# Optimization experiments

Measured on AMD Instinct MI355X. Metric: run time of the kernel, lower is better.

Reference implementation:

```python
import jax, jax.numpy as jnp
import numpy as np
import math

N_EMBD = 64
HEAD_SIZE = 64
B, T = 16, 2048


def setup_inputs() -> dict:
    key = jax.random.key(0)
    k1, k2, k3, k4 = jax.random.split(key, 4)
    inputs = jax.random.normal(k1, (B, T, N_EMBD), dtype=jnp.float32)
    # Causal mask: True where attention is NOT allowed (upper triangle),
    # matching masked_fill_(mask, -1e9) with mask = ~tril.
    mask = jnp.triu(jnp.ones((T, T), dtype=bool), k=1)
    # nn.Linear(n_embd, head_size, bias=False) weights, stored as
    # (n_embd, head_size) so projection is inputs @ W (== x @ W_torch.T).
    scale = 1.0 / math.sqrt(N_EMBD)
    Wq = jax.random.uniform(k2, (N_EMBD, HEAD_SIZE), jnp.float32, -scale, scale)
    Wk = jax.random.uniform(k3, (N_EMBD, HEAD_SIZE), jnp.float32, -scale, scale)
    Wv = jax.random.uniform(k4, (N_EMBD, HEAD_SIZE), jnp.float32, -scale, scale)
    return {"inputs": inputs, "mask": mask, "Wq": Wq, "Wk": Wk, "Wv": Wv}


def reference(inputs, mask, Wq, Wk, Wv):
    # inputs: (B, T, n_embd); mask: (T, T) bool broadcast over batch
    q = inputs @ Wq  # (B, T, H)
    k = inputs @ Wk  # (B, T, H)
    v = inputs @ Wv  # (B, T, H)
    inv_sqrt_h = 1.0 / math.sqrt(HEAD_SIZE)
    scores = jnp.einsum('bth,bsh->bts', q, k) * inv_sqrt_h  # (B, T, T)
    scores = jnp.where(mask, jnp.float32(-1e9), scores)
    attention = jax.nn.softmax(scores, axis=-1)
    out = jnp.einsum('bts,bsh->bth', attention, v)  # (B, T, H)
    return out
```

## Files before the change

### kernel.cpp

```cpp
#include <hip/hip_runtime.h>
#include <stdint.h>


typedef __bf16 bf16x8 __attribute__((ext_vector_type(8)));
typedef __bf16 bf16x4 __attribute__((ext_vector_type(4)));
typedef float f32x4 __attribute__((ext_vector_type(4)));

#define QSCALE 0.18033688011112042f

#if __has_builtin(__builtin_amdgcn_exp2f)
#define EXP2(x) __builtin_amdgcn_exp2f(x)
#else
#define EXP2(x) exp2f(x)
#endif

__device__ __forceinline__ unsigned short f2bf(float f) {
  union { float f; unsigned u; } x; x.f = f;
  unsigned r = x.u + 0x7fffu + ((x.u >> 16) & 1u);
  return (unsigned short)(r >> 16);
}

__device__ __forceinline__ int swz(int row, int bytecol) {
  return row * 128 + (bytecol ^ ((row & 7) << 4));
}
__device__ __forceinline__ bf16x8 frag(const unsigned short* base, int row, int kf, int lane) {
  int off = swz(row, kf * 64 + ((lane >> 4) << 4));
  return *(const bf16x8*)((const char*)base + off);
}

__global__ __launch_bounds__(256, 2) void proj_kernel(
    const float* __restrict__ X, const float* __restrict__ Wq,
    const float* __restrict__ Wk, const float* __restrict__ Wv,
    unsigned short* __restrict__ Qg, unsigned short* __restrict__ Kg,
    unsigned short* __restrict__ Vtg) {
  __shared__ __align__(16) unsigned short Xs[128 * 64];
  __shared__ __align__(16) unsigned short Ws[3 * 64 * 64];
  const int tid = threadIdx.x, lane = tid & 63, w = tid >> 6;
  const long grow0 = (long)blockIdx.x * 128;

  for (int c = tid; c < 1024; c += 256) {
    int r = c >> 3, cc = c & 7;
    const float* src = X + (grow0 + r) * 64 + cc * 8;
    float4 f0 = *(const float4*)src;
    float4 f1 = *(const float4*)(src + 4);
    uint4 d;
    d.x = f2bf(f0.x) | ((unsigned)f2bf(f0.y) << 16);
    d.y = f2bf(f0.z) | ((unsigned)f2bf(f0.w) << 16);
    d.z = f2bf(f1.x) | ((unsigned)f2bf(f1.y) << 16);
    d.w = f2bf(f1.z) | ((unsigned)f2bf(f1.w) << 16);
    *(uint4*)((char*)Xs + swz(r, cc * 16)) = d;
  }
  for (int c = tid; c < 3 * 4096; c += 256) {
    const int mat = c >> 12;
    const int rr = c & 4095;
    const int e = rr >> 6, hh = rr & 63;
    const float* wsrc = (mat == 0) ? Wq : (mat == 1) ? Wk : Wv;
    *(unsigned short*)((char*)(Ws + mat * 4096) + swz(hh, e * 2)) = f2bf(wsrc[e * 64 + hh]);
  }
  __syncthreads();

  const f32x4 zero = {0.f, 0.f, 0.f, 0.f};
  const int mrowb = w * 32;

  bf16x8 xf[2][2];
#pragma unroll
  for (int s = 0; s < 2; ++s)
#pragma unroll
    for (int kf = 0; kf < 2; ++kf)
      xf[s][kf] = frag(Xs, mrowb + s * 16 + (lane & 15), kf, lane);

#pragma unroll
  for (int mat = 0; mat < 2; ++mat) {
    unsigned short* dst = mat ? Kg : Qg;
    const unsigned short* wbase = Ws + mat * 4096;
#pragma unroll
    for (int s = 0; s < 2; ++s) {
#pragma unroll
      for (int nt = 0; nt < 4; ++nt) {
        bf16x8 b0 = frag(wbase, nt * 16 + (lane & 15), 0, lane);
        bf16x8 b1 = frag(wbase, nt * 16 + (lane & 15), 1, lane);
        f32x4 acc = __builtin_amdgcn_mfma_f32_16x16x32_bf16(xf[s][0], b0, zero, 0, 0, 0);
        acc = __builtin_amdgcn_mfma_f32_16x16x32_bf16(xf[s][1], b1, acc, 0, 0, 0);
        long row0 = grow0 + mrowb + s * 16 + ((lane >> 4) << 2);
        int col = nt * 16 + (lane & 15);
#pragma unroll
        for (int i = 0; i < 4; ++i) {
          float v = acc[i];
          if (mat == 0) v *= QSCALE;
          dst[(row0 + i) * 64 + col] = f2bf(v);
        }
      }
    }
  }

  const unsigned short* wv = Ws + 2 * 4096;
  const int b = (int)(grow0 >> 11);
  const int tin0 = (int)(grow0 & 2047);
#pragma unroll
  for (int mt = 0; mt < 4; ++mt) {
    bf16x8 a0 = frag(wv, mt * 16 + (lane & 15), 0, lane);
    bf16x8 a1 = frag(wv, mt * 16 + (lane & 15), 1, lane);
#pragma unroll
    for (int s = 0; s < 2; ++s) {
      f32x4 acc = __builtin_amdgcn_mfma_f32_16x16x32_bf16(a0, xf[s][0], zero, 0, 0, 0);
      acc = __builtin_amdgcn_mfma_f32_16x16x32_bf16(a1, xf[s][1], acc, 0, 0, 0);
      int t = tin0 + mrowb + s * 16 + (lane & 15);
      int h0 = mt * 16 + ((lane >> 4) << 2);
#pragma unroll
      for (int i = 0; i < 4; ++i)
        Vtg[((long)(b * 64 + h0 + i)) * 2048 + t] = f2bf(acc[i]);
    }
  }
}

__global__ __launch_bounds__(256, 4) void attn3_kernel(
    const unsigned short* __restrict__ Qg, const unsigned short* __restrict__ Kg,
    const unsigned short* __restrict__ Vtg, float* __restrict__ Og) {
  __shared__ __align__(16) unsigned char smem[32768];

  const int bid = blockIdx.x;
  const int slot = bid >> 3;
  const int b = ((bid & 7) << 1) + (slot & 1);
  const int j = slot >> 1;
  const int qt = (j & 1) ? (j >> 1) : 63 - (j >> 1);
  const int q0 = qt * 32;

  const int tid = threadIdx.x;
  const int lane = tid & 63, w = tid >> 6;
  const int g = lane >> 4, ln = lane & 15;
  const int h = w & 1, qs = w >> 1;

  const int ns = (q0 + 95) >> 6;

  const unsigned short* qrow = Qg + ((long)b * 2048 + q0 + qs * 16 + ln) * 64;
  const bf16x8 qb0 = *(const bf16x8*)(qrow + g * 8);
  const bf16x8 qb1 = *(const bf16x8*)(qrow + 32 + g * 8);

  const unsigned short* kbase = Kg + (long)b * 2048 * 64;
  const unsigned short* vbase = Vtg + (long)b * 64 * 2048;

  const int sr = tid >> 2;
  const int sc = tid & 3;

  const f32x4 zero = {0.f, 0.f, 0.f, 0.f};
  f32x4 oacc[4];
#pragma unroll
  for (int nt = 0; nt < 4; ++nt) oacc[nt] = zero;
  float den = 0.f;

  {
    const unsigned short* kg = kbase + (long)sr * 64 + sc * 16;
    uint4 k0 = *(const uint4*)kg;
    uint4 k1 = *(const uint4*)(kg + 8);
    const unsigned short* vg = vbase + (long)sr * 2048 + sc * 16;
    uint4 v0 = *(const uint4*)vg;
    uint4 v1 = *(const uint4*)(vg + 8);
    unsigned short* Kb = (unsigned short*)smem;
    unsigned short* Vb = (unsigned short*)(smem + 8192);
    *(uint4*)((char*)Kb + swz(sr, sc * 32)) = k0;
    *(uint4*)((char*)Kb + swz(sr, sc * 32 + 16)) = k1;
    *(uint4*)((char*)Vb + swz(sr, sc * 32)) = v0;
    *(uint4*)((char*)Vb + swz(sr, sc * 32 + 16)) = v1;
  }
  __syncthreads();

  int cur = 0;
  for (int t = 0; t < ns; ++t) {
    const bool pre = (t + 1 < ns);
    uint4 k0, k1, v0, v1;
    if (pre) {
      const int kv0n = (t + 1) * 64;
      const unsigned short* kg = kbase + (long)(kv0n + sr) * 64 + sc * 16;
      k0 = *(const uint4*)kg;
      k1 = *(const uint4*)(kg + 8);
      const unsigned short* vg = vbase + (long)sr * 2048 + kv0n + sc * 16;
      v0 = *(const uint4*)vg;
      v1 = *(const uint4*)(vg + 8);
    }

    const unsigned short* Kb = (const unsigned short*)(smem + cur * 16384);
    const unsigned short* Vb = (const unsigned short*)(smem + cur * 16384 + 8192);

    bf16x8 ka00 = frag(Kb, h * 32 + ln,      0, lane);
    bf16x8 ka01 = frag(Kb, h * 32 + ln,      1, lane);
    bf16x8 ka10 = frag(Kb, h * 32 + 16 + ln, 0, lane);
    bf16x8 ka11 = frag(Kb, h * 32 + 16 + ln, 1, lane);

    bf16x8 vb[4];
#pragma unroll
    for (int nt = 0; nt < 4; ++nt) {
      int row = nt * 16 + ln;
      bf16x4 lo = *(const bf16x4*)((const char*)Vb + swz(row, h * 64 + g * 8));
      bf16x4 hi = *(const bf16x4*)((const char*)Vb + swz(row, h * 64 + 32 + g * 8));
      vb[nt] = __builtin_shufflevector(lo, hi, 0, 1, 2, 3, 4, 5, 6, 7);
    }

    __builtin_amdgcn_s_setprio(1);
    f32x4 st0 = __builtin_amdgcn_mfma_f32_16x16x32_bf16(ka00, qb0, zero, 0, 0, 0);
    st0 = __builtin_amdgcn_mfma_f32_16x16x32_bf16(ka01, qb1, st0, 0, 0, 0);
    f32x4 st1 = __builtin_amdgcn_mfma_f32_16x16x32_bf16(ka10, qb0, zero, 0, 0, 0);
    st1 = __builtin_amdgcn_mfma_f32_16x16x32_bf16(ka11, qb1, st1, 0, 0, 0);
    __builtin_amdgcn_s_setprio(0);

    if (t == ns - 1) {
      const int qglob = q0 + qs * 16 + ln;
      const int kvb = t * 64 + h * 32 + g * 4;
#pragma unroll
      for (int i = 0; i < 4; ++i) {
        if (kvb + i > qglob) st0[i] = -1e30f;
        if (kvb + 16 + i > qglob) st1[i] = -1e30f;
      }
    }

    bf16x8 pa;
#pragma unroll
    for (int i = 0; i < 4; ++i) {
      float p0 = EXP2(st0[i]);
      float p1 = EXP2(st1[i]);
      den += p0 + p1;
      pa[i] = (__bf16)p0;
      pa[4 + i] = (__bf16)p1;
    }

    __builtin_amdgcn_s_setprio(1);
#pragma unroll
    for (int nt = 0; nt < 4; ++nt)
      oacc[nt] = __builtin_amdgcn_mfma_f32_16x16x32_bf16(pa, vb[nt], oacc[nt], 0, 0, 0);
    __builtin_amdgcn_s_setprio(0);

    if (pre) {
      unsigned short* Kn = (unsigned short*)(smem + (cur ^ 1) * 16384);
      unsigned short* Vn = (unsigned short*)(smem + (cur ^ 1) * 16384 + 8192);
      *(uint4*)((char*)Kn + swz(sr, sc * 32)) = k0;
      *(uint4*)((char*)Kn + swz(sr, sc * 32 + 16)) = k1;
      *(uint4*)((char*)Vn + swz(sr, sc * 32)) = v0;
      *(uint4*)((char*)Vn + swz(sr, sc * 32 + 16)) = v1;
    }
    __syncthreads();
    cur ^= 1;
  }

  den += __shfl_xor(den, 16);
  den += __shfl_xor(den, 32);

  float* Olds = (float*)smem;
  float* Dlds = (float*)(smem + 4 * 16 * 68 * 4);
#pragma unroll
  for (int nt = 0; nt < 4; ++nt)
#pragma unroll
    for (int i = 0; i < 4; ++i)
      Olds[(w * 16 + g * 4 + i) * 68 + nt * 16 + ln] = oacc[nt][i];
  if (lane < 16) Dlds[w * 16 + ln] = den;
  __syncthreads();

  const int q32 = tid >> 3;
  const int r = q32 & 15, qsx = q32 >> 4;
  const int d0 = (tid & 7) * 8;
  float dd = Dlds[(qsx * 2) * 16 + r] + Dlds[(qsx * 2 + 1) * 16 + r];
  float inv = 1.0f / dd;
  float acc[8];
#pragma unroll
  for (int e = 0; e < 8; ++e)
    acc[e] = (Olds[((qsx * 2) * 16 + r) * 68 + d0 + e] +
              Olds[((qsx * 2 + 1) * 16 + r) * 68 + d0 + e]) * inv;
  float* outp = Og + ((long)b * 2048 + q0 + q32) * 64 + d0;
  *(float4*)outp = make_float4(acc[0], acc[1], acc[2], acc[3]);
  *(float4*)(outp + 4) = make_float4(acc[4], acc[5], acc[6], acc[7]);
}

extern "C" void kernel_launch(void* const* d_in, const int* in_sizes, int n_in,
                              void* d_out, int out_size, void* d_ws, size_t ws_size,
                              hipStream_t stream) {
  const float* X  = (const float*)d_in[0];
  const float* Wq = (const float*)d_in[2];
  const float* Wk = (const float*)d_in[3];
  const float* Wv = (const float*)d_in[4];

  unsigned short* Qg  = (unsigned short*)d_ws;
  unsigned short* Kg  = Qg + 2097152;
  unsigned short* Vtg = Kg + 2097152;

  proj_kernel<<<256, 256, 0, stream>>>(X, Wq, Wk, Wv, Qg, Kg, Vtg);
  attn3_kernel<<<1024, 256, 0, stream>>>(Qg, Kg, Vtg, (float*)d_out);
}
```

Before: 46.67 us.

## Split KV range across waves with per-wave async K loads and split projection grid

The attention kernel now gives each wave its own strided subset of 32-key tiles, covering all 32 queries, instead of splitting by query half and key half. K tiles are staged with per-wave global_load_lds double buffering and V is read straight from global memory into registers, which drops the block-wide __syncthreads in the loop. Partial outputs and denominators from the four waves are merged through LDS at the end. The projection kernel runs one block per weight matrix (grid y=3) for more parallelism, at the cost of converting X three times. The exp2 builtin is also replaced by exp2f. Risks include uncoalesced V loads and hand-set vmcnt waits.

```diff
diff --git a/kernel.cpp b/kernel.cpp
--- a/kernel.cpp
+++ b/kernel.cpp
@@ -7,12 +7,6 @@
 typedef float f32x4 __attribute__((ext_vector_type(4)));
 
 #define QSCALE 0.18033688011112042f
-
-#if __has_builtin(__builtin_amdgcn_exp2f)
-#define EXP2(x) __builtin_amdgcn_exp2f(x)
-#else
-#define EXP2(x) exp2f(x)
-#endif
 
 __device__ __forceinline__ unsigned short f2bf(float f) {
   union { float f; unsigned u; } x; x.f = f;
@@ -28,14 +22,21 @@
   return *(const bf16x8*)((const char*)base + off);
 }
 
-__global__ __launch_bounds__(256, 2) void proj_kernel(
+__device__ __forceinline__ void gload_lds16(const unsigned short* g, unsigned short* l) {
+  __builtin_amdgcn_global_load_lds(
+      (const __attribute__((address_space(1))) unsigned int*)g,
+      (__attribute__((address_space(3))) unsigned int*)l, 16, 0, 0);
+}
+
+__global__ __launch_bounds__(256, 3) void proj_kernel(
     const float* __restrict__ X, const float* __restrict__ Wq,
     const float* __restrict__ Wk, const float* __restrict__ Wv,
     unsigned short* __restrict__ Qg, unsigned short* __restrict__ Kg,
     unsigned short* __restrict__ Vtg) {
   __shared__ __align__(16) unsigned short Xs[128 * 64];
-  __shared__ __align__(16) unsigned short Ws[3 * 64 * 64];
+  __shared__ __align__(16) unsigned short Ws[64 * 64];
   const int tid = threadIdx.x, lane = tid & 63, w = tid >> 6;
+  const int mat = blockIdx.y;
   const long grow0 = (long)blockIdx.x * 128;
 
   for (int c = tid; c < 1024; c += 256) {
@@ -50,12 +51,10 @@
     d.w = f2bf(f1.z) | ((unsigned)f2bf(f1.w) << 16);
     *(uint4*)((char*)Xs + swz(r, cc * 16)) = d;
   }
-  for (int c = tid; c < 3 * 4096; c += 256) {
-    const int mat = c >> 12;
-    const int rr = c & 4095;
-    const int e = rr >> 6, hh = rr & 63;
-    const float* wsrc = (mat == 0) ? Wq : (mat == 1) ? Wk : Wv;
-    *(unsigned short*)((char*)(Ws + mat * 4096) + swz(hh, e * 2)) = f2bf(wsrc[e * 64 + hh]);
+  const float* wsrc = (mat == 0) ? Wq : (mat == 1) ? Wk : Wv;
+  for (int c = tid; c < 4096; c += 256) {
+    int e = c >> 6, hh = c & 63;
+    *(unsigned short*)((char*)Ws + swz(hh, e * 2)) = f2bf(wsrc[c]);
   }
   __syncthreads();
 
@@ -69,16 +68,14 @@
     for (int kf = 0; kf < 2; ++kf)
       xf[s][kf] = frag(Xs, mrowb + s * 16 + (lane & 15), kf, lane);
 
-#pragma unroll
-  for (int mat = 0; mat < 2; ++mat) {
+  if (mat < 2) {
     unsigned short* dst = mat ? Kg : Qg;
-    const unsigned short* wbase = Ws + mat * 4096;
 #pragma unroll
     for (int s = 0; s < 2; ++s) {
 #pragma unroll
       for (int nt = 0; nt < 4; ++nt) {
-        bf16x8 b0 = frag(wbase, nt * 16 + (lane & 15), 0, lane);
-        bf16x8 b1 = frag(wbase, nt * 16 + (lane & 15), 1, lane);
+        bf16x8 b0 = frag(Ws, nt * 16 + (lane & 15), 0, lane);
+        bf16x8 b1 = frag(Ws, nt * 16 + (lane & 15), 1, lane);
         f32x4 acc = __builtin_amdgcn_mfma_f32_16x16x32_bf16(xf[s][0], b0, zero, 0, 0, 0);
         acc = __builtin_amdgcn_mfma_f32_16x16x32_bf16(xf[s][1], b1, acc, 0, 0, 0);
         long row0 = grow0 + mrowb + s * 16 + ((lane >> 4) << 2);
@@ -91,32 +88,31 @@
         }
       }
     }
-  }
-
-  const unsigned short* wv = Ws + 2 * 4096;
-  const int b = (int)(grow0 >> 11);
-  const int tin0 = (int)(grow0 & 2047);
-#pragma unroll
-  for (int mt = 0; mt < 4; ++mt) {
-    bf16x8 a0 = frag(wv, mt * 16 + (lane & 15), 0, lane);
-    bf16x8 a1 = frag(wv, mt * 16 + (lane & 15), 1, lane);
-#pragma unroll
-    for (int s = 0; s < 2; ++s) {
-      f32x4 acc = __builtin_amdgcn_mfma_f32_16x16x32_bf16(a0, xf[s][0], zero, 0, 0, 0);
-      acc = __builtin_amdgcn_mfma_f32_16x16x32_bf16(a1, xf[s][1], acc, 0, 0, 0);
-      int t = tin0 + mrowb + s * 16 + (lane & 15);
-      int h0 = mt * 16 + ((lane >> 4) << 2);
-#pragma unroll
-      for (int i = 0; i < 4; ++i)
-        Vtg[((long)(b * 64 + h0 + i)) * 2048 + t] = f2bf(acc[i]);
-    }
-  }
-}
-
-__global__ __launch_bounds__(256, 4) void attn3_kernel(
+  } else {
+    const int b = (int)(grow0 >> 11);
+    const int tin0 = (int)(grow0 & 2047);
+#pragma unroll
+    for (int mt = 0; mt < 4; ++mt) {
+      bf16x8 a0 = frag(Ws, mt * 16 + (lane & 15), 0, lane);
+      bf16x8 a1 = frag(Ws, mt * 16 + (lane & 15), 1, lane);
+#pragma unroll
+      for (int s = 0; s < 2; ++s) {
+        f32x4 acc = __builtin_amdgcn_mfma_f32_16x16x32_bf16(a0, xf[s][0], zero, 0, 0, 0);
+        acc = __builtin_amdgcn_mfma_f32_16x16x32_bf16(a1, xf[s][1], acc, 0, 0, 0);
+        int t = tin0 + mrowb + s * 16 + (lane & 15);
+        int h0 = mt * 16 + ((lane >> 4) << 2);
+#pragma unroll
+        for (int i = 0; i < 4; ++i)
+          Vtg[((long)(b * 64 + h0 + i)) * 2048 + t] = f2bf(acc[i]);
+      }
+    }
+  }
+}
+
+__global__ __launch_bounds__(256, 4) void attn4_kernel(
     const unsigned short* __restrict__ Qg, const unsigned short* __restrict__ Kg,
     const unsigned short* __restrict__ Vtg, float* __restrict__ Og) {
-  __shared__ __align__(16) unsigned char smem[32768];
+  __shared__ __align__(16) unsigned char smem[35840];
 
   const int bid = blockIdx.x;
   const int slot = bid >> 3;
@@ -128,141 +124,149 @@
   const int tid = threadIdx.x;
   const int lane = tid & 63, w = tid >> 6;
   const int g = lane >> 4, ln = lane & 15;
-  const int h = w & 1, qs = w >> 1;
-
-  const int ns = (q0 + 95) >> 6;
-
-  const unsigned short* qrow = Qg + ((long)b * 2048 + q0 + qs * 16 + ln) * 64;
-  const bf16x8 qb0 = *(const bf16x8*)(qrow + g * 8);
-  const bf16x8 qb1 = *(const bf16x8*)(qrow + 32 + g * 8);
+
+  const int ntiles = qt + 1;
+
+  const unsigned short* qrow = Qg + ((long)b * 2048 + q0) * 64;
+  const bf16x8 qb00 = *(const bf16x8*)(qrow + ln * 64 + g * 8);
+  const bf16x8 qb01 = *(const bf16x8*)(qrow + ln * 64 + 32 + g * 8);
+  const bf16x8 qb10 = *(const bf16x8*)(qrow + (16 + ln) * 64 + g * 8);
+  const bf16x8 qb11 = *(const bf16x8*)(qrow + (16 + ln) * 64 + 32 + g * 8);
 
   const unsigned short* kbase = Kg + (long)b * 2048 * 64;
   const unsigned short* vbase = Vtg + (long)b * 64 * 2048;
-
-  const int sr = tid >> 2;
-  const int sc = tid & 3;
+  unsigned short* Klds = (unsigned short*)(smem + w * 8192);
+
+  const int koff = ((lane >> 3) << 6) + (((lane & 7) << 3) ^ ((lane >> 3) << 3));
 
   const f32x4 zero = {0.f, 0.f, 0.f, 0.f};
-  f32x4 oacc[4];
-#pragma unroll
-  for (int nt = 0; nt < 4; ++nt) oacc[nt] = zero;
-  float den = 0.f;
-
-  {
-    const unsigned short* kg = kbase + (long)sr * 64 + sc * 16;
-    uint4 k0 = *(const uint4*)kg;
-    uint4 k1 = *(const uint4*)(kg + 8);
-    const unsigned short* vg = vbase + (long)sr * 2048 + sc * 16;
-    uint4 v0 = *(const uint4*)vg;
-    uint4 v1 = *(const uint4*)(vg + 8);
-    unsigned short* Kb = (unsigned short*)smem;
-    unsigned short* Vb = (unsigned short*)(smem + 8192);
-    *(uint4*)((char*)Kb + swz(sr, sc * 32)) = k0;
-    *(uint4*)((char*)Kb + swz(sr, sc * 32 + 16)) = k1;
-    *(uint4*)((char*)Vb + swz(sr, sc * 32)) = v0;
-    *(uint4*)((char*)Vb + swz(sr, sc * 32 + 16)) = v1;
-  }
+  f32x4 oacc0[4], oacc1[4];
+#pragma unroll
+  for (int nt = 0; nt < 4; ++nt) { oacc0[nt] = zero; oacc1[nt] = zero; }
+  float den0 = 0.f, den1 = 0.f;
+
+  int cur = 0;
+  if (w < ntiles) {
+    const unsigned short* kg = kbase + (long)(w * 32) * 64 + koff;
+#pragma unroll
+    for (int i = 0; i < 4; ++i)
+      gload_lds16(kg + i * 512, Klds + i * 512);
+  }
+
+  for (int t = w; t < ntiles; t += 4) {
+    const int kv0 = t * 32;
+    const bool pre = (t + 4 < ntiles);
+    if (pre) {
+      const unsigned short* kg = kbase + (long)((t + 4) * 32) * 64 + koff;
+#pragma unroll
+      for (int i = 0; i < 4; ++i)
+        gload_lds16(kg + i * 512, Klds + (cur ^ 1) * 2048 + i * 512);
+    }
+    bf16x4 vlo0, vlo1, vlo2, vlo3, vhi0, vhi1, vhi2, vhi3;
+    {
+      const unsigned short* vr0 = vbase + (long)ln * 2048 + kv0 + g * 4;
+      const unsigned short* vr1 = vr0 + 16 * 2048;
+      const unsigned short* vr2 = vr1 + 16 * 2048;
+      const unsigned short* vr3 = vr2 + 16 * 2048;
+      vlo0 = *(const bf16x4*)vr0;  vhi0 = *(const bf16x4*)(vr0 + 16);
+      vlo1 = *(const bf16x4*)vr1;  vhi1 = *(const bf16x4*)(vr1 + 16);
+      vlo2 = *(const bf16x4*)vr2;  vhi2 = *(const bf16x4*)(vr2 + 16);
+      vlo3 = *(const bf16x4*)vr3;  vhi3 = *(const bf16x4*)(vr3 + 16);
+    }
+    if (pre) asm volatile("s_waitcnt vmcnt(12)" ::: "memory");
+    else     asm volatile("s_waitcnt vmcnt(8)" ::: "memory");
+
+    const unsigned short* Kb = Klds + cur * 2048;
+    bf16x8 ka00 = frag(Kb, ln, 0, lane);
+    bf16x8 ka01 = frag(Kb, ln, 1, lane);
+    bf16x8 ka10 = frag(Kb, 16 + ln, 0, lane);
+    bf16x8 ka11 = frag(Kb, 16 + ln, 1, lane);
+
+    __builtin_amdgcn_s_setprio(1);
+    f32x4 st00 = __builtin_amdgcn_mfma_f32_16x16x32_bf16(ka00, qb00, zero, 0, 0, 0);
+    st00 = __builtin_amdgcn_mfma_f32_16x16x32_bf16(ka01, qb01, st00, 0, 0, 0);
+    f32x4 st01 = __builtin_amdgcn_mfma_f32_16x16x32_bf16(ka00, qb10, zero, 0, 0, 0);
+    st01 = __builtin_amdgcn_mfma_f32_16x16x32_bf16(ka01, qb11, st01, 0, 0, 0);
+    f32x4 st10 = __builtin_amdgcn_mfma_f32_16x16x32_bf16(ka10, qb00, zero, 0, 0, 0);
+    st10 = __builtin_amdgcn_mfma_f32_16x16x32_bf16(ka11, qb01, st10, 0, 0, 0);
+    f32x4 st11 = __builtin_amdgcn_mfma_f32_16x16x32_bf16(ka10, qb10, zero, 0, 0, 0);
+    st11 = __builtin_amdgcn_mfma_f32_16x16x32_bf16(ka11, qb11, st11, 0, 0, 0);
+    __builtin_amdgcn_s_setprio(0);
+
+    if (t == ntiles - 1) {
+      const int qg0 = q0 + ln, qg1 = q0 + 16 + ln;
+      const int kvb = kv0 + g * 4;
+#pragma unroll
+      for (int i = 0; i < 4; ++i) {
+        if (kvb + i > qg0)      st00[i] = -1e30f;
+        if (kvb + i > qg1)      st01[i] = -1e30f;
+        if (kvb + 16 + i > qg0) st10[i] = -1e30f;
+        if (kvb + 16 + i > qg1) st11[i] = -1e30f;
+      }
+    }
+
+    bf16x8 pa0, pa1;
+#pragma unroll
+    for (int i = 0; i < 4; ++i) {
+      float p00 = exp2f(st00[i]);
+      float p01 = exp2f(st01[i]);
+      float p10 = exp2f(st10[i]);
+      float p11 = exp2f(st11[i]);
+      den0 += p00 + p10;
+      den1 += p01 + p11;
+      pa0[i] = (__bf16)p00;  pa0[4 + i] = (__bf16)p10;
+      pa1[i] = (__bf16)p01;  pa1[4 + i] = (__bf16)p11;
+    }
+
+    __builtin_amdgcn_s_setprio(1);
+    {
+      bf16x8 vb = __builtin_shufflevector(vlo0, vhi0, 0, 1, 2, 3, 4, 5, 6, 7);
+      oacc0[0] = __builtin_amdgcn_mfma_f32_16x16x32_bf16(pa0, vb, oacc0[0], 0, 0, 0);
+      oacc1[0] = __builtin_amdgcn_mfma_f32_16x16x32_bf16(pa1, vb, oacc1[0], 0, 0, 0);
+      vb = __builtin_shufflevector(vlo1, vhi1, 0, 1, 2, 3, 4, 5, 6, 7);
+      oacc0[1] = __builtin_amdgcn_mfma_f32_16x16x32_bf16(pa0, vb, oacc0[1], 0, 0, 0);
+      oacc1[1] = __builtin_amdgcn_mfma_f32_16x16x32_bf16(pa1, vb, oacc1[1], 0, 0, 0);
+      vb = __builtin_shufflevector(vlo2, vhi2, 0, 1, 2, 3, 4, 5, 6, 7);
+      oacc0[2] = __builtin_amdgcn_mfma_f32_16x16x32_bf16(pa0, vb, oacc0[2], 0, 0, 0);
+      oacc1[2] = __builtin_amdgcn_mfma_f32_16x16x32_bf16(pa1, vb, oacc1[2], 0, 0, 0);
+      vb = __builtin_shufflevector(vlo3, vhi3, 0, 1, 2, 3, 4, 5, 6, 7);
+      oacc0[3] = __builtin_amdgcn_mfma_f32_16x16x32_bf16(pa0, vb, oacc0[3], 0, 0, 0);
+      oacc1[3] = __builtin_amdgcn_mfma_f32_16x16x32_bf16(pa1, vb, oacc1[3], 0, 0, 0);
+    }
+    __builtin_amdgcn_s_setprio(0);
+    cur ^= 1;
+  }
+
+  den0 += __shfl_xor(den0, 16);
+  den0 += __shfl_xor(den0, 32);
+  den1 += __shfl_xor(den1, 16);
+  den1 += __shfl_xor(den1, 32);
+
   __syncthreads();
-
-  int cur = 0;
-  for (int t = 0; t < ns; ++t) {
-    const bool pre = (t + 1 < ns);
-    uint4 k0, k1, v0, v1;
-    if (pre) {
-      const int kv0n = (t + 1) * 64;
-      const unsigned short* kg = kbase + (long)(kv0n + sr) * 64 + sc * 16;
-      k0 = *(const uint4*)kg;
-      k1 = *(const uint4*)(kg + 8);
-      const unsigned short* vg = vbase + (long)sr * 2048 + kv0n + sc * 16;
-      v0 = *(const uint4*)vg;
-      v1 = *(const uint4*)(vg + 8);
-    }
-
-    const unsigned short* Kb = (const unsigned short*)(smem + cur * 16384);
-    const unsigned short* Vb = (const unsigned short*)(smem + cur * 16384 + 8192);
-
-    bf16x8 ka00 = frag(Kb, h * 32 + ln,      0, lane);
-    bf16x8 ka01 = frag(Kb, h * 32 + ln,      1, lane);
-    bf16x8 ka10 = frag(Kb, h * 32 + 16 + ln, 0, lane);
-    bf16x8 ka11 = frag(Kb, h * 32 + 16 + ln, 1, lane);
-
-    bf16x8 vb[4];
-#pragma unroll
-    for (int nt = 0; nt < 4; ++nt) {
-      int row = nt * 16 + ln;
-      bf16x4 lo = *(const bf16x4*)((const char*)Vb + swz(row, h * 64 + g * 8));
-      bf16x4 hi = *(const bf16x4*)((const char*)Vb + swz(row, h * 64 + 32 + g * 8));
-      vb[nt] = __builtin_shufflevector(lo, hi, 0, 1, 2, 3, 4, 5, 6, 7);
-    }
-
-    __builtin_amdgcn_s_setprio(1);
-    f32x4 st0 = __builtin_amdgcn_mfma_f32_16x16x32_bf16(ka00, qb0, zero, 0, 0, 0);
-    st0 = __builtin_amdgcn_mfma_f32_16x16x32_bf16(ka01, qb1, st0, 0, 0, 0);
-    f32x4 st1 = __builtin_amdgcn_mfma_f32_16x16x32_bf16(ka10, qb0, zero, 0, 0, 0);
-    st1 = __builtin_amdgcn_mfma_f32_16x16x32_bf16(ka11, qb1, st1, 0, 0, 0);
-    __builtin_amdgcn_s_setprio(0);
-
-    if (t == ns - 1) {
-      const int qglob = q0 + qs * 16 + ln;
-      const int kvb = t * 64 + h * 32 + g * 4;
-#pragma unroll
-      for (int i = 0; i < 4; ++i) {
-        if (kvb + i > qglob) st0[i] = -1e30f;
-        if (kvb + 16 + i > qglob) st1[i] = -1e30f;
-      }
-    }
-
-    bf16x8 pa;
+  float* Olds = (float*)smem;
+  float* Dlds = (float*)(smem + 34816);
+#pragma unroll
+  for (int nt = 0; nt < 4; ++nt)
 #pragma unroll
     for (int i = 0; i < 4; ++i) {
-      float p0 = EXP2(st0[i]);
-      float p1 = EXP2(st1[i]);
-      den += p0 + p1;
-      pa[i] = (__bf16)p0;
-      pa[4 + i] = (__bf16)p1;
-    }
-
-    __builtin_amdgcn_s_setprio(1);
-#pragma unroll
-    for (int nt = 0; nt < 4; ++nt)
-      oacc[nt] = __builtin_amdgcn_mfma_f32_16x16x32_bf16(pa, vb[nt], oacc[nt], 0, 0, 0);
-    __builtin_amdgcn_s_setprio(0);
-
-    if (pre) {
-      unsigned short* Kn = (unsigned short*)(smem + (cur ^ 1) * 16384);
-      unsigned short* Vn = (unsigned short*)(smem + (cur ^ 1) * 16384 + 8192);
-      *(uint4*)((char*)Kn + swz(sr, sc * 32)) = k0;
-      *(uint4*)((char*)Kn + swz(sr, sc * 32 + 16)) = k1;
-      *(uint4*)((char*)Vn + swz(sr, sc * 32)) = v0;
-      *(uint4*)((char*)Vn + swz(sr, sc * 32 + 16)) = v1;
-    }
-    __syncthreads();
-    cur ^= 1;
-  }
-
-  den += __shfl_xor(den, 16);
-  den += __shfl_xor(den, 32);
-
-  float* Olds = (float*)smem;
-  float* Dlds = (float*)(smem + 4 * 16 * 68 * 4);
-#pragma unroll
-  for (int nt = 0; nt < 4; ++nt)
-#pragma unroll
-    for (int i = 0; i < 4; ++i)
-      Olds[(w * 16 + g * 4 + i) * 68 + nt * 16 + ln] = oacc[nt][i];
-  if (lane < 16) Dlds[w * 16 + ln] = den;
+      Olds[(w * 32 + g * 4 + i) * 68 + nt * 16 + ln] = oacc0[nt][i];
+      Olds[(w * 32 + 16 + g * 4 + i) * 68 + nt * 16 + ln] = oacc1[nt][i];
+    }
+  if (lane < 16) {
+    Dlds[w * 32 + ln] = den0;
+    Dlds[w * 32 + 16 + ln] = den1;
+  }
   __syncthreads();
 
   const int q32 = tid >> 3;
-  const int r = q32 & 15, qsx = q32 >> 4;
   const int d0 = (tid & 7) * 8;
-  float dd = Dlds[(qsx * 2) * 16 + r] + Dlds[(qsx * 2 + 1) * 16 + r];
+  float dd = Dlds[q32] + Dlds[32 + q32] + Dlds[64 + q32] + Dlds[96 + q32];
   float inv = 1.0f / dd;
   float acc[8];
 #pragma unroll
   for (int e = 0; e < 8; ++e)
-    acc[e] = (Olds[((qsx * 2) * 16 + r) * 68 + d0 + e] +
-              Olds[((qsx * 2 + 1) * 16 + r) * 68 + d0 + e]) * inv;
+    acc[e] = (Olds[q32 * 68 + d0 + e] + Olds[(32 + q32) * 68 + d0 + e] +
+              Olds[(64 + q32) * 68 + d0 + e] + Olds[(96 + q32) * 68 + d0 + e]) * inv;
   float* outp = Og + ((long)b * 2048 + q0 + q32) * 64 + d0;
   *(float4*)outp = make_float4(acc[0], acc[1], acc[2], acc[3]);
   *(float4*)(outp + 4) = make_float4(acc[4], acc[5], acc[6], acc[7]);
@@ -280,6 +284,6 @@
   unsigned short* Kg  = Qg + 2097152;
   unsigned short* Vtg = Kg + 2097152;
 
-  proj_kernel<<<256, 256, 0, stream>>>(X, Wq, Wk, Wv, Qg, Kg, Vtg);
-  attn3_kernel<<<1024, 256, 0, stream>>>(Qg, Kg, Vtg, (float*)d_out);
-}
+  proj_kernel<<<dim3(256, 3), 256, 0, stream>>>(X, Wq, Wk, Wv, Qg, Kg, Vtg);
+  attn4_kernel<<<1024, 256, 0, stream>>>(Qg, Kg, Vtg, (float*)d_out);
+}
```

Result: slower. 70.88 us (+51.9%).
